# Kernel optimization log

Measured on AMD Instinct MI355X. Metric: run time of the kernel, lower is better.

## Reference

```python
import jax, jax.numpy as jnp
import numpy as np
from jax import lax

B = 16384
NWIRES = 4


def _conv(x, w, b):
    # NCHW conv, stride 1, SAME padding (pad 1 for k=3)
    y = lax.conv_general_dilated(x, w, (1, 1), ((1, 1), (1, 1)),
                                 dimension_numbers=("NCHW", "OIHW", "NCHW"))
    return y + b[None, :, None, None]


def _pool2(x):
    b, c, h, w = x.shape
    return x.reshape(b, c, h // 2, 2, w // 2, 2).max(axis=(3, 5))


def _apply_1q(state, U, wire):
    # state: (B,2,2,2,2) complex; U: (B,2,2) complex
    s = jnp.moveaxis(state, wire + 1, -1)
    s = jnp.einsum("bij,b...j->b...i", U, s)
    return jnp.moveaxis(s, -1, wire + 1)


def _apply_cnot(state, c, t):
    s0 = jnp.take(state, 0, axis=c + 1)
    s1 = jnp.take(state, 1, axis=c + 1)
    ta = t + 1 if t < c else t  # target axis index after removing control axis
    s1 = jnp.flip(s1, axis=ta)
    return jnp.stack([s0, s1], axis=c + 1)


def _ry(th):
    c = jnp.cos(th / 2)
    s = jnp.sin(th / 2)
    U = jnp.stack([jnp.stack([c, -s], -1), jnp.stack([s, c], -1)], -2)
    return U.astype(jnp.complex64)


def _rz(th):
    e = jnp.exp(-0.5j * th.astype(jnp.complex64))
    z = jnp.zeros_like(e)
    return jnp.stack([jnp.stack([e, z], -1), jnp.stack([z, jnp.conj(e)], -1)], -2)


def _rx(th):
    c = jnp.cos(th / 2).astype(jnp.complex64)
    s = jnp.sin(th / 2).astype(jnp.complex64)
    return jnp.stack([jnp.stack([c, -1j * s], -1), jnp.stack([-1j * s, c], -1)], -2)


def _circuit(params):
    # params: (B, 16) -> PauliZ expvals (B, 4)
    b = params.shape[0]
    state = jnp.zeros((b, 16), jnp.complex64).at[:, 0].set(1.0).reshape(b, 2, 2, 2, 2)
    for i in range(NWIRES):
        state = _apply_1q(state, _ry(params[:, 4 * i + 0]), i)
        state = _apply_1q(state, _rz(params[:, 4 * i + 1]), i)
        state = _apply_1q(state, _rx(params[:, 4 * i + 2]), i)
        state = _apply_cnot(state, i, (i + 1) % NWIRES)
    probs = state.real ** 2 + state.imag ** 2  # (B,2,2,2,2)
    zs = []
    for i in range(NWIRES):
        p = probs.sum(axis=tuple(a for a in range(1, 5) if a != i + 1))  # (B,2)
        zs.append(p[:, 0] - p[:, 1])
    return jnp.stack(zs, axis=-1)


def setup_inputs() -> dict:
    key = jax.random.key(0)
    ks = jax.random.split(key, 12)
    d = {}
    d["x"] = jax.random.normal(ks[0], (B, 1, 28, 28), jnp.float32)
    d["conv1_w"] = jax.random.normal(ks[1], (4, 1, 3, 3), jnp.float32) * 0.3
    d["conv1_b"] = jax.random.normal(ks[2], (4,), jnp.float32) * 0.1
    d["conv2_w"] = jax.random.normal(ks[3], (4, 4, 3, 3), jnp.float32) * 0.15
    d["conv2_b"] = jax.random.normal(ks[4], (4,), jnp.float32) * 0.1
    d["pl_w"] = jax.random.normal(ks[5], (16, 196), jnp.float32) * 0.07
    d["pl_b"] = jax.random.normal(ks[6], (16,), jnp.float32) * 0.05
    d["ro_w"] = jax.random.normal(ks[7], (4, 4), jnp.float32) * 0.5
    d["ro_b"] = jax.random.normal(ks[8], (4,), jnp.float32) * 0.1
    d["bn_w"] = jnp.ones((4,), jnp.float32)
    d["bn_b"] = jnp.zeros((4,), jnp.float32)
    return d


def reference(x, conv1_w, conv1_b, conv2_w, conv2_b, pl_w, pl_b, ro_w, ro_b, bn_w, bn_b):
    h = _pool2(jax.nn.relu(_conv(x, conv1_w, conv1_b)))   # (B,4,14,14)
    h = _pool2(jax.nn.relu(_conv(h, conv2_w, conv2_b)))   # (B,4,7,7)
    flat = h.reshape(x.shape[0], -1)                      # (B,196)
    params = flat @ pl_w.T + pl_b                         # (B,16)
    z = _circuit(params)                                  # (B,4)
    out = z @ ro_w.T + ro_b                               # (B,4)
    mean = out.mean(0)
    var = out.var(0)  # biased, matches torch BN training normalization
    return (out - mean) / jnp.sqrt(var + 1e-5) * bn_w + bn_b
```

## Files before the change

### kernel.cpp

```cpp
#include <hip/hip_runtime.h>
#include <math.h>

#define BATCH 16384

typedef float v2f __attribute__((ext_vector_type(2)));

__device__ __forceinline__ v2f pk_fma(v2f a, v2f b, v2f c) {
  return __builtin_elementwise_fma(a, b, c);
}
__device__ __forceinline__ v2f pk_max(v2f a, v2f b) {
  return __builtin_elementwise_max(a, b);
}

__global__ __launch_bounds__(256) void qnat_fused(
    const float* __restrict__ x,
    const float* __restrict__ w1,
    const float* __restrict__ b1,
    const float* __restrict__ w2,
    const float* __restrict__ b2,
    const float* __restrict__ plw,
    const float* __restrict__ plb,
    const float* __restrict__ rw,
    const float* __restrict__ rb,
    float* __restrict__ pre,
    float* __restrict__ stats)
{
  __shared__ __align__(16) float h1p[4][4 * 288 + 16];
  __shared__ __align__(16) float h2[4][212];
  __shared__ __align__(16) float plw_s[16 * 196];
  __shared__ float s_red[4][8];

  const int tid = threadIdx.x;
  const int w = tid >> 6;
  const int lane = tid & 63;
  const int wid = blockIdx.x * 4 + w;
  const int base = wid * 4;

  {
    float4* dst = (float4*)plw_s;
    const float4* src = (const float4*)plw;
    #pragma unroll
    for (int t = 0; t < 4; t++) dst[t * 256 + tid] = src[t * 256 + tid];
    if (tid < 784 - 1024 + 256) {}
    if (tid < 16) dst[768 + tid] = src[768 + tid];
  }

  {
    float4 z4 = make_float4(0.f, 0.f, 0.f, 0.f);
    float4* hz = (float4*)&h1p[w][0];
    #pragma unroll
    for (int t = 0; t < 5; t++) {
      int p = t * 64 + lane;
      if (p < 292) hz[p] = z4;
    }
  }
  __syncthreads();

  const int i = lane >> 2;
  const int q = lane & 3;
  const bool c1act = lane < 56;

  float4 pfa[4], pfb[4];
  #pragma unroll
  for (int r = 0; r < 4; r++) { pfa[r] = make_float4(0,0,0,0); pfb[r] = make_float4(0,0,0,0); }

  if (c1act) {
    const float* xb = x + (size_t)base * 784;
    #pragma unroll
    for (int r = 0; r < 4; r++) {
      int row = 2 * i - 1 + r;
      if (0 <= row && row < 28) {
        const float* rp = xb + row * 28;
        pfa[r] = *(const float4*)(rp + 8 * q);
        if (q < 3) pfb[r] = *(const float4*)(rp + 8 * q + 4);
      }
    }
  }

  float as0 = 0.f, as1 = 0.f, as2 = 0.f, as3 = 0.f;
  float aq0 = 0.f, aq1 = 0.f, aq2 = 0.f, aq3 = 0.f;

  for (int it = 0; it < 4; ++it) {
    const int sample = base + it;

    if (c1act) {
      const float* xb = x + (size_t)sample * 784;
      float win[4][10];
      #pragma unroll
      for (int r = 0; r < 4; r++) {
        int row = 2 * i - 1 + r;
        bool v = (0 <= row && row < 28);
        const float* rp = xb + row * 28;
        win[r][0] = (v && q > 0) ? rp[8 * q - 1] : 0.0f;
        win[r][1] = pfa[r].x; win[r][2] = pfa[r].y;
        win[r][3] = pfa[r].z; win[r][4] = pfa[r].w;
        win[r][5] = pfb[r].x; win[r][6] = pfb[r].y;
        win[r][7] = pfb[r].z; win[r][8] = pfb[r].w;
        win[r][9] = (v && q < 3) ? rp[8 * q + 8] : 0.0f;
      }
      if (it != 3) {
        const float* xn = x + (size_t)(sample + 1) * 784;
        #pragma unroll
        for (int r = 0; r < 4; r++) {
          int row = 2 * i - 1 + r;
          pfa[r] = make_float4(0,0,0,0);
          pfb[r] = make_float4(0,0,0,0);
          if (0 <= row && row < 28) {
            const float* rp = xn + row * 28;
            pfa[r] = *(const float4*)(rp + 8 * q);
            if (q < 3) pfb[r] = *(const float4*)(rp + 8 * q + 4);
          }
        }
      }
      v2f P[4][9];
      #pragma unroll
      for (int r = 0; r < 4; r++)
        #pragma unroll
        for (int k = 0; k < 9; k++) P[r][k] = (v2f){win[r][k], win[r][k + 1]};

      float* hb = &h1p[w][18 * (i + 1) + 1 + 4 * q];
      #pragma unroll
      for (int c = 0; c < 4; c++) {
        const float* wc = w1 + c * 9;
        const v2f bias2 = (v2f){b1[c], b1[c]};
        v2f a0[4], a1[4];
        #pragma unroll
        for (int jj = 0; jj < 4; jj++) { a0[jj] = bias2; a1[jj] = bias2; }
        #pragma unroll
        for (int dy = 0; dy < 3; dy++)
          #pragma unroll
          for (int dx = 0; dx < 3; dx++) {
            const float wv = wc[dy * 3 + dx];
            const v2f wvv = (v2f){wv, wv};
            #pragma unroll
            for (int jj = 0; jj < 4; jj++) {
              a0[jj] = pk_fma(P[dy][2 * jj + dx],     wvv, a0[jj]);
              a1[jj] = pk_fma(P[dy + 1][2 * jj + dx], wvv, a1[jj]);
            }
          }
        float m[4];
        #pragma unroll
        for (int jj = 0; jj < 4; jj++) {
          v2f mm = pk_max(a0[jj], a1[jj]);
          m[jj] = fmaxf(fmaxf(mm.x, mm.y), 0.0f);
        }
        float* p = hb + 288 * c;
        if (q < 3) {
          p[0] = m[0];
          *(float2*)(p + 1) = make_float2(m[1], m[2]);
          p[3] = m[3];
        } else {
          p[0] = m[0];
          p[1] = m[1];
        }
      }
    }

    {
      const int jq = lane & 7;
      const int i2 = lane >> 3;
      if (i2 < 7 && jq < 7) {
        v2f acc[4][2];
        #pragma unroll
        for (int co = 0; co < 4; co++) {
          const v2f bb = (v2f){b2[co], b2[co]};
          acc[co][0] = bb; acc[co][1] = bb;
        }
        #pragma unroll
        for (int ci = 0; ci < 4; ci++) {
          const float* rp = &h1p[w][288 * ci + 36 * i2 + 2 * jq];
          v2f Q[4][3];
          #pragma unroll
          for (int r = 0; r < 4; r++) {
            v2f a = *(const v2f*)(rp + 18 * r);
            v2f b = *(const v2f*)(rp + 18 * r + 2);
            Q[r][0] = a;
            Q[r][1] = (v2f){a.y, b.x};
            Q[r][2] = b;
          }
          #pragma unroll
          for (int co = 0; co < 4; co++) {
            const float* wp = w2 + (co * 4 + ci) * 9;
            #pragma unroll
            for (int dy = 0; dy < 3; dy++)
              #pragma unroll
              for (int dx = 0; dx < 3; dx++) {
                const float wv = wp[dy * 3 + dx];
                const v2f wvv = (v2f){wv, wv};
                acc[co][0] = pk_fma(Q[dy][dx],     wvv, acc[co][0]);
                acc[co][1] = pk_fma(Q[dy + 1][dx], wvv, acc[co][1]);
              }
          }
        }
        #pragma unroll
        for (int co = 0; co < 4; co++) {
          v2f mm = pk_max(acc[co][0], acc[co][1]);
          h2[w][52 * co + 7 * i2 + jq] = fmaxf(fmaxf(mm.x, mm.y), 0.0f);
        }
      }
    }

    float cv = 0.0f, sv = 0.0f;
    {
      const int k = lane & 15;
      const int part = lane >> 4;
      const float* hh = &h2[w][52 * part];
      const float* wp = &plw_s[k * 196 + part * 49];
      v2f s2 = (v2f){0.0f, 0.0f};
      #pragma unroll
      for (int t = 0; t < 12; t++) {
        float4 hv = *(const float4*)(hh + 4 * t);
        float4 wv = *(const float4*)(wp + 4 * t);
        s2 = pk_fma((v2f){hv.x, hv.y}, (v2f){wv.x, wv.y}, s2);
        s2 = pk_fma((v2f){hv.z, hv.w}, (v2f){wv.z, wv.w}, s2);
      }
      float s = fmaf(hh[48], wp[48], s2.x + s2.y);
      s += __shfl_down(s, 32, 64);
      s += __shfl_down(s, 16, 64);
      if (lane < 16) {
        float pv = s + plb[k];
        __sincosf(pv * 0.5f, &sv, &cv);
      }
    }

    if (lane < 16) {
      const int l = lane;
      float re = (l == 0) ? 1.0f : 0.0f;
      float im = 0.0f;
      #pragma unroll
      for (int qi = 0; qi < 4; qi++) {
        const int beta = 3 - qi;
        const int m = 1 << beta;
        const int b = (l >> beta) & 1;
        float c = __shfl(cv, 4 * qi, 64), s = __shfl(sv, 4 * qi, 64);
        float pr_ = __shfl_xor(re, m, 64), pi_ = __shfl_xor(im, m, 64);
        float sg = b ? s : -s;
        re = fmaf(c, re, sg * pr_);
        im = fmaf(c, im, sg * pi_);
        c = __shfl(cv, 4 * qi + 1, 64); s = __shfl(sv, 4 * qi + 1, 64);
        float sz = b ? s : -s;
        float nr = c * re - sz * im;
        float ni = c * im + sz * re;
        re = nr; im = ni;
        c = __shfl(cv, 4 * qi + 2, 64); s = __shfl(sv, 4 * qi + 2, 64);
        pr_ = __shfl_xor(re, m, 64); pi_ = __shfl_xor(im, m, 64);
        nr = fmaf(c, re, s * pi_);
        ni = fmaf(c, im, -s * pr_);
        re = nr; im = ni;
        const int tm = 1 << (3 - ((qi + 1) & 3));
        float fr = __shfl_xor(re, tm, 64), fi = __shfl_xor(im, tm, 64);
        if (b) { re = fr; im = fi; }
      }
      float pr2 = re * re + im * im;
      float z0 = ((l >> 3) & 1) ? -pr2 : pr2;
      float z1 = ((l >> 2) & 1) ? -pr2 : pr2;
      float z2 = ((l >> 1) & 1) ? -pr2 : pr2;
      float z3 = (l & 1) ? -pr2 : pr2;
      #pragma unroll
      for (int off = 8; off >= 1; off >>= 1) {
        z0 += __shfl_xor(z0, off, 64);
        z1 += __shfl_xor(z1, off, 64);
        z2 += __shfl_xor(z2, off, 64);
        z3 += __shfl_xor(z3, off, 64);
      }
      if (l == 0) {
        float o0 = fmaf(rw[0],  z0, fmaf(rw[1],  z1, fmaf(rw[2],  z2, fmaf(rw[3],  z3, rb[0]))));
        float o1 = fmaf(rw[4],  z0, fmaf(rw[5],  z1, fmaf(rw[6],  z2, fmaf(rw[7],  z3, rb[1]))));
        float o2 = fmaf(rw[8],  z0, fmaf(rw[9],  z1, fmaf(rw[10], z2, fmaf(rw[11], z3, rb[2]))));
        float o3 = fmaf(rw[12], z0, fmaf(rw[13], z1, fmaf(rw[14], z2, fmaf(rw[15], z3, rb[3]))));
        *(float4*)(pre + (size_t)sample * 4) = make_float4(o0, o1, o2, o3);
        as0 += o0; aq0 += o0 * o0;
        as1 += o1; aq1 += o1 * o1;
        as2 += o2; aq2 += o2 * o2;
        as3 += o3; aq3 += o3 * o3;
      }
    }
  }

  if (lane == 0) {
    s_red[w][0] = as0; s_red[w][4] = aq0;
    s_red[w][1] = as1; s_red[w][5] = aq1;
    s_red[w][2] = as2; s_red[w][6] = aq2;
    s_red[w][3] = as3; s_red[w][7] = aq3;
  }
  __syncthreads();
  if (tid < 8) {
    float v = s_red[0][tid] + s_red[1][tid] + s_red[2][tid] + s_red[3][tid];
    atomicAdd(&stats[tid], v);
  }
}

__global__ __launch_bounds__(256) void qnat_bn(
    float* __restrict__ pre,
    const float* __restrict__ stats,
    const float* __restrict__ bnw,
    const float* __restrict__ bnb)
{
  int idx = blockIdx.x * 256 + threadIdx.x;
  int c = idx & 3;
  float mean = stats[c] * (1.0f / BATCH);
  float ex2 = stats[4 + c] * (1.0f / BATCH);
  float var = ex2 - mean * mean;
  float inv = rsqrtf(var + 1e-5f);
  pre[idx] = (pre[idx] - mean) * inv * bnw[c] + bnb[c];
}

extern "C" void kernel_launch(void* const* d_in, const int* in_sizes, int n_in,
                              void* d_out, int out_size, void* d_ws, size_t ws_size,
                              hipStream_t stream) {
  const float* x   = (const float*)d_in[0];
  const float* w1  = (const float*)d_in[1];
  const float* b1  = (const float*)d_in[2];
  const float* w2  = (const float*)d_in[3];
  const float* b2  = (const float*)d_in[4];
  const float* plw = (const float*)d_in[5];
  const float* plb = (const float*)d_in[6];
  const float* rw  = (const float*)d_in[7];
  const float* rb  = (const float*)d_in[8];
  const float* bnw = (const float*)d_in[9];
  const float* bnb = (const float*)d_in[10];

  float* out   = (float*)d_out;
  float* stats = (float*)d_ws;

  hipMemsetAsync(stats, 0, 8 * sizeof(float), stream);
  qnat_fused<<<BATCH / 16, 256, 0, stream>>>(x, w1, b1, w2, b2, plw, plb, rw, rb, out, stats);
  qnat_bn<<<(BATCH * 4) / 256, 256, 0, stream>>>(out, stats, bnw, bnb);
}
```

Baseline: 146.9 us.

## Batch linear layer and quantum circuit across four samples per wavefront

```diff
diff --git a/kernel.cpp b/kernel.cpp
--- a/kernel.cpp
+++ b/kernel.cpp
@@ -26,8 +26,7 @@
     float* __restrict__ stats)
 {
   __shared__ __align__(16) float h1p[4][4 * 288 + 16];
-  __shared__ __align__(16) float h2[4][212];
-  __shared__ __align__(16) float plw_s[16 * 196];
+  __shared__ __align__(16) float h2[4][4][196];
   __shared__ float s_red[4][8];
 
   const int tid = threadIdx.x;
@@ -37,15 +36,6 @@
   const int base = wid * 4;
 
   {
-    float4* dst = (float4*)plw_s;
-    const float4* src = (const float4*)plw;
-    #pragma unroll
-    for (int t = 0; t < 4; t++) dst[t * 256 + tid] = src[t * 256 + tid];
-    if (tid < 784 - 1024 + 256) {}
-    if (tid < 16) dst[768 + tid] = src[768 + tid];
-  }
-
-  {
     float4 z4 = make_float4(0.f, 0.f, 0.f, 0.f);
     float4* hz = (float4*)&h1p[w][0];
     #pragma unroll
@@ -54,7 +44,6 @@
       if (p < 292) hz[p] = z4;
     }
   }
-  __syncthreads();
 
   const int i = lane >> 2;
   const int q = lane & 3;
@@ -76,9 +65,6 @@
       }
     }
   }
-
-  float as0 = 0.f, as1 = 0.f, as2 = 0.f, as3 = 0.f;
-  float aq0 = 0.f, aq1 = 0.f, aq2 = 0.f, aq3 = 0.f;
 
   for (int it = 0; it < 4; ++it) {
     const int sample = base + it;
@@ -195,93 +181,98 @@
         #pragma unroll
         for (int co = 0; co < 4; co++) {
           v2f mm = pk_max(acc[co][0], acc[co][1]);
-          h2[w][52 * co + 7 * i2 + jq] = fmaxf(fmaxf(mm.x, mm.y), 0.0f);
-        }
-      }
-    }
-
-    float cv = 0.0f, sv = 0.0f;
-    {
-      const int k = lane & 15;
-      const int part = lane >> 4;
-      const float* hh = &h2[w][52 * part];
-      const float* wp = &plw_s[k * 196 + part * 49];
-      v2f s2 = (v2f){0.0f, 0.0f};
-      #pragma unroll
-      for (int t = 0; t < 12; t++) {
-        float4 hv = *(const float4*)(hh + 4 * t);
-        float4 wv = *(const float4*)(wp + 4 * t);
-        s2 = pk_fma((v2f){hv.x, hv.y}, (v2f){wv.x, wv.y}, s2);
-        s2 = pk_fma((v2f){hv.z, hv.w}, (v2f){wv.z, wv.w}, s2);
-      }
-      float s = fmaf(hh[48], wp[48], s2.x + s2.y);
-      s += __shfl_down(s, 32, 64);
-      s += __shfl_down(s, 16, 64);
-      if (lane < 16) {
-        float pv = s + plb[k];
-        __sincosf(pv * 0.5f, &sv, &cv);
-      }
-    }
-
-    if (lane < 16) {
-      const int l = lane;
-      float re = (l == 0) ? 1.0f : 0.0f;
-      float im = 0.0f;
-      #pragma unroll
-      for (int qi = 0; qi < 4; qi++) {
-        const int beta = 3 - qi;
-        const int m = 1 << beta;
-        const int b = (l >> beta) & 1;
-        float c = __shfl(cv, 4 * qi, 64), s = __shfl(sv, 4 * qi, 64);
-        float pr_ = __shfl_xor(re, m, 64), pi_ = __shfl_xor(im, m, 64);
-        float sg = b ? s : -s;
-        re = fmaf(c, re, sg * pr_);
-        im = fmaf(c, im, sg * pi_);
-        c = __shfl(cv, 4 * qi + 1, 64); s = __shfl(sv, 4 * qi + 1, 64);
-        float sz = b ? s : -s;
-        float nr = c * re - sz * im;
-        float ni = c * im + sz * re;
-        re = nr; im = ni;
-        c = __shfl(cv, 4 * qi + 2, 64); s = __shfl(sv, 4 * qi + 2, 64);
-        pr_ = __shfl_xor(re, m, 64); pi_ = __shfl_xor(im, m, 64);
-        nr = fmaf(c, re, s * pi_);
-        ni = fmaf(c, im, -s * pr_);
-        re = nr; im = ni;
-        const int tm = 1 << (3 - ((qi + 1) & 3));
-        float fr = __shfl_xor(re, tm, 64), fi = __shfl_xor(im, tm, 64);
-        if (b) { re = fr; im = fi; }
-      }
-      float pr2 = re * re + im * im;
-      float z0 = ((l >> 3) & 1) ? -pr2 : pr2;
-      float z1 = ((l >> 2) & 1) ? -pr2 : pr2;
-      float z2 = ((l >> 1) & 1) ? -pr2 : pr2;
-      float z3 = (l & 1) ? -pr2 : pr2;
-      #pragma unroll
-      for (int off = 8; off >= 1; off >>= 1) {
-        z0 += __shfl_xor(z0, off, 64);
-        z1 += __shfl_xor(z1, off, 64);
-        z2 += __shfl_xor(z2, off, 64);
-        z3 += __shfl_xor(z3, off, 64);
-      }
-      if (l == 0) {
-        float o0 = fmaf(rw[0],  z0, fmaf(rw[1],  z1, fmaf(rw[2],  z2, fmaf(rw[3],  z3, rb[0]))));
-        float o1 = fmaf(rw[4],  z0, fmaf(rw[5],  z1, fmaf(rw[6],  z2, fmaf(rw[7],  z3, rb[1]))));
-        float o2 = fmaf(rw[8],  z0, fmaf(rw[9],  z1, fmaf(rw[10], z2, fmaf(rw[11], z3, rb[2]))));
-        float o3 = fmaf(rw[12], z0, fmaf(rw[13], z1, fmaf(rw[14], z2, fmaf(rw[15], z3, rb[3]))));
-        *(float4*)(pre + (size_t)sample * 4) = make_float4(o0, o1, o2, o3);
-        as0 += o0; aq0 += o0 * o0;
-        as1 += o1; aq1 += o1 * o1;
-        as2 += o2; aq2 += o2 * o2;
-        as3 += o3; aq3 += o3 * o3;
-      }
-    }
-  }
-
-  if (lane == 0) {
-    s_red[w][0] = as0; s_red[w][4] = aq0;
-    s_red[w][1] = as1; s_red[w][5] = aq1;
-    s_red[w][2] = as2; s_red[w][6] = aq2;
-    s_red[w][3] = as3; s_red[w][7] = aq3;
+          h2[w][it][49 * co + 7 * i2 + jq] = fmaxf(fmaxf(mm.x, mm.y), 0.0f);
+        }
+      }
+    }
+  }
+
+  const int s2 = lane >> 4;
+  const int k = lane & 15;
+
+  float cv, sv;
+  {
+    const float4* hv4 = (const float4*)&h2[w][s2][0];
+    const float4* wv4 = (const float4*)(plw + k * 196);
+    v2f sacc = (v2f){0.0f, 0.0f};
+    #pragma unroll 7
+    for (int t = 0; t < 49; t++) {
+      float4 hv = hv4[t];
+      float4 wv = wv4[t];
+      sacc = pk_fma((v2f){hv.x, hv.y}, (v2f){wv.x, wv.y}, sacc);
+      sacc = pk_fma((v2f){hv.z, hv.w}, (v2f){wv.z, wv.w}, sacc);
+    }
+    float pv = sacc.x + sacc.y + plb[k];
+    __sincosf(pv * 0.5f, &sv, &cv);
+  }
+
+  {
+    const int l = k;
+    const int gb = lane & 48;
+    float re = (l == 0) ? 1.0f : 0.0f;
+    float im = 0.0f;
+    #pragma unroll
+    for (int qi = 0; qi < 4; qi++) {
+      const int beta = 3 - qi;
+      const int m = 1 << beta;
+      const int b = (l >> beta) & 1;
+      float c = __shfl(cv, gb + 4 * qi, 64), s = __shfl(sv, gb + 4 * qi, 64);
+      float pr_ = __shfl_xor(re, m, 64), pi_ = __shfl_xor(im, m, 64);
+      float sg = b ? s : -s;
+      re = fmaf(c, re, sg * pr_);
+      im = fmaf(c, im, sg * pi_);
+      c = __shfl(cv, gb + 4 * qi + 1, 64); s = __shfl(sv, gb + 4 * qi + 1, 64);
+      float sz = b ? s : -s;
+      float nr = c * re - sz * im;
+      float ni = c * im + sz * re;
+      re = nr; im = ni;
+      c = __shfl(cv, gb + 4 * qi + 2, 64); s = __shfl(sv, gb + 4 * qi + 2, 64);
+      pr_ = __shfl_xor(re, m, 64); pi_ = __shfl_xor(im, m, 64);
+      nr = fmaf(c, re, s * pi_);
+      ni = fmaf(c, im, -s * pr_);
+      re = nr; im = ni;
+      const int tm = 1 << (3 - ((qi + 1) & 3));
+      float fr = __shfl_xor(re, tm, 64), fi = __shfl_xor(im, tm, 64);
+      if (b) { re = fr; im = fi; }
+    }
+    float pr2 = re * re + im * im;
+    float z0 = ((l >> 3) & 1) ? -pr2 : pr2;
+    float z1 = ((l >> 2) & 1) ? -pr2 : pr2;
+    float z2 = ((l >> 1) & 1) ? -pr2 : pr2;
+    float z3 = (l & 1) ? -pr2 : pr2;
+    #pragma unroll
+    for (int off = 8; off >= 1; off >>= 1) {
+      z0 += __shfl_xor(z0, off, 64);
+      z1 += __shfl_xor(z1, off, 64);
+      z2 += __shfl_xor(z2, off, 64);
+      z3 += __shfl_xor(z3, off, 64);
+    }
+    float as0 = 0.f, as1 = 0.f, as2 = 0.f, as3 = 0.f;
+    float aq0 = 0.f, aq1 = 0.f, aq2 = 0.f, aq3 = 0.f;
+    if (l == 0) {
+      float o0 = fmaf(rw[0],  z0, fmaf(rw[1],  z1, fmaf(rw[2],  z2, fmaf(rw[3],  z3, rb[0]))));
+      float o1 = fmaf(rw[4],  z0, fmaf(rw[5],  z1, fmaf(rw[6],  z2, fmaf(rw[7],  z3, rb[1]))));
+      float o2 = fmaf(rw[8],  z0, fmaf(rw[9],  z1, fmaf(rw[10], z2, fmaf(rw[11], z3, rb[2]))));
+      float o3 = fmaf(rw[12], z0, fmaf(rw[13], z1, fmaf(rw[14], z2, fmaf(rw[15], z3, rb[3]))));
+      *(float4*)(pre + (size_t)(base + s2) * 4) = make_float4(o0, o1, o2, o3);
+      as0 = o0; aq0 = o0 * o0;
+      as1 = o1; aq1 = o1 * o1;
+      as2 = o2; aq2 = o2 * o2;
+      as3 = o3; aq3 = o3 * o3;
+    }
+    #pragma unroll
+    for (int off = 32; off >= 16; off >>= 1) {
+      as0 += __shfl_down(as0, off, 64); aq0 += __shfl_down(aq0, off, 64);
+      as1 += __shfl_down(as1, off, 64); aq1 += __shfl_down(aq1, off, 64);
+      as2 += __shfl_down(as2, off, 64); aq2 += __shfl_down(aq2, off, 64);
+      as3 += __shfl_down(as3, off, 64); aq3 += __shfl_down(aq3, off, 64);
+    }
+    if (lane == 0) {
+      s_red[w][0] = as0; s_red[w][4] = aq0;
+      s_red[w][1] = as1; s_red[w][5] = aq1;
+      s_red[w][2] = as2; s_red[w][6] = aq2;
+      s_red[w][3] = as3; s_red[w][7] = aq3;
+    }
   }
   __syncthreads();
   if (tid < 8) {
```

Result: faster. 138.2 us (-5.9%).
